# Optimization experiments

Measured on AMD Instinct MI355X. Metric: run time of the kernel, lower is better.

## Reference

```python
import jax, jax.numpy as jnp
import numpy as np

N_NODES = 50000
N_EDGES = 150000
D_FEAT = 512
HIDDEN = 512
N_CLASSES = 47


def gcn_conv(x, edge_index, W, b, n_nodes):
    """PyG GCNConv: out = D^{-1/2} (A + I) D^{-1/2} (x @ W) + b."""
    h = x @ W  # [N, out_dim] dense GEMM
    loop = jnp.arange(n_nodes, dtype=edge_index.dtype)
    row = jnp.concatenate([edge_index[0], loop])  # source
    col = jnp.concatenate([edge_index[1], loop])  # target
    ones = jnp.ones(row.shape[0], dtype=h.dtype)
    deg = jax.ops.segment_sum(ones, col, num_segments=n_nodes)  # in-degree + 1
    dinv = jnp.where(deg > 0, jax.lax.rsqrt(deg), 0.0)
    norm = dinv[row] * dinv[col]  # [E+N]
    msg = norm[:, None] * h[row]  # gather + scale
    out = jax.ops.segment_sum(msg, col, num_segments=n_nodes)  # scatter-add
    return out + b


def setup_inputs() -> dict:
    key = jax.random.key(0)
    k1, k2, k3, k4, k5, k6 = jax.random.split(key, 6)
    x = jax.random.normal(k1, (N_NODES, D_FEAT), dtype=jnp.float32)
    edge_index = jax.random.randint(k2, (2, N_EDGES), 0, N_NODES, dtype=jnp.int64)
    s1 = (6.0 / (D_FEAT + HIDDEN)) ** 0.5
    s2 = (6.0 / (HIDDEN + N_CLASSES)) ** 0.5
    W1 = jax.random.uniform(k3, (D_FEAT, HIDDEN), jnp.float32, -s1, s1)
    b1 = jnp.zeros((HIDDEN,), jnp.float32)
    W2 = jax.random.uniform(k4, (HIDDEN, N_CLASSES), jnp.float32, -s2, s2)
    b2 = jnp.zeros((N_CLASSES,), jnp.float32)
    return {"x": x, "edge_index": edge_index, "W1": W1, "b1": b1, "W2": W2, "b2": b2}


def reference(x, edge_index, W1, b1, W2, b2):
    n = x.shape[0]
    h = gcn_conv(x, edge_index, W1, b1, n)
    h = jax.nn.relu(h)
    # F.dropout(p=0.5, training=self.training): eval mode -> identity
    out = gcn_conv(h, edge_index, W2, b2, n)
    return out
```

## Files before the change

kernel.cpp:

```cpp
#include <hip/hip_runtime.h>
#include <hip/hip_bf16.h>

#define NNODES 50000
#define NEDGES 150000
#define DFEAT  512
#define HID    512
#define NCLS   47

typedef __hip_bfloat16 bf16;
typedef __attribute__((ext_vector_type(8))) short short8;
typedef __attribute__((ext_vector_type(4))) float float4v;

typedef const __attribute__((address_space(1))) unsigned int* gas_t;
typedef __attribute__((address_space(3))) unsigned int* las_t;
__device__ __forceinline__ void load_lds16(const void* g, void* l) {
    __builtin_amdgcn_global_load_lds((gas_t)g, (las_t)l, 16, 0, 0);
}

__device__ __forceinline__ float bfbits_lo(unsigned int w) {
    return __uint_as_float((w & 0xFFFFu) << 16);
}
__device__ __forceinline__ float bfbits_hi(unsigned int w) {
    return __uint_as_float(w & 0xFFFF0000u);
}

__global__ void k_detect(const void* x, const void* ei, int* flags) {
    __shared__ int scnt[64], sor[64];
    int t = threadIdx.x;
    const unsigned short* xs = (const unsigned short*)x;
    int c = 0;
    for (int i = t; i < 256; i += 64) {
        unsigned int e = (xs[2 * i] >> 7) & 0xFF;
        c += (e >= 117 && e <= 130) ? 1 : 0;
    }
    const int* w = (const int*)ei;
    int o = 0;
    for (int i = 2 * t + 1; i < 512; i += 128) o |= w[i];
    scnt[t] = c; sor[t] = o;
    __syncthreads();
    if (t == 0) {
        int C = 0, O = 0;
        for (int i = 0; i < 64; i++) { C += scnt[i]; O |= sor[i]; }
        flags[0] = (C > 128) ? 1 : 0;
        flags[1] = (O == 0) ? 1 : 0;
    }
}

__device__ __forceinline__ int eidx(const void* ei, int half, int e, int is64) {
    if (is64) return (int)((const long long*)ei)[(size_t)half * NEDGES + e];
    return ((const int*)ei)[half * NEDGES + e];
}

__global__ void k_zero32(unsigned int* p, size_t n) {
    size_t i = (size_t)blockIdx.x * blockDim.x + threadIdx.x;
    if (i < n) p[i] = 0u;
}

__global__ void k_cvt(const void* src, float* dst, int n, const int* flags) {
    int i = blockIdx.x * blockDim.x + threadIdx.x;
    if (i >= n) return;
    dst[i] = flags[0] ? __bfloat162float(((const bf16*)src)[i]) : ((const float*)src)[i];
}

__global__ void k_cvt_w1t(const void* W1, bf16* W1T, const int* flags) {
    int i = blockIdx.x * blockDim.x + threadIdx.x;
    if (i >= DFEAT * HID) return;
    int k = i / HID, n = i % HID;
    float v = flags[0] ? __bfloat162float(((const bf16*)W1)[i]) : ((const float*)W1)[i];
    W1T[(size_t)n * DFEAT + k] = __float2bfloat16(v);
}

__global__ void k_cvt_w2t(const void* W2, bf16* W2T, const int* flags) {
    int i = blockIdx.x * blockDim.x + threadIdx.x;
    if (i >= 64 * HID) return;
    int n = i / HID, k = i % HID;
    float v = 0.0f;
    if (n < NCLS) {
        size_t idx = (size_t)k * NCLS + n;
        v = flags[0] ? __bfloat162float(((const bf16*)W2)[idx]) : ((const float*)W2)[idx];
    }
    W2T[(size_t)n * HID + k] = __float2bfloat16(v);
}

__global__ void k_count(const void* ei, int* cnt, const int* flags) {
    int e = blockIdx.x * blockDim.x + threadIdx.x;
    if (e >= NEDGES) return;
    atomicAdd(&cnt[eidx(ei, 1, e, flags[1])], 1);
}

__global__ void k_dinv(const int* cnt, float* dinv) {
    int i = blockIdx.x * blockDim.x + threadIdx.x;
    if (i < NNODES) dinv[i] = rsqrtf(1.0f + (float)cnt[i]);
}

__global__ __launch_bounds__(256) void k_scan_part(const int* cnt, int* part) {
    __shared__ int s[256];
    int i = blockIdx.x * 256 + threadIdx.x;
    s[threadIdx.x] = (i < NNODES) ? cnt[i] : 0;
    __syncthreads();
    for (int off = 128; off > 0; off >>= 1) {
        if (threadIdx.x < off) s[threadIdx.x] += s[threadIdx.x + off];
        __syncthreads();
    }
    if (threadIdx.x == 0) part[blockIdx.x] = s[0];
}

__global__ __launch_bounds__(256) void k_scan_off(int* part, int n) {
    __shared__ int s[256];
    int v = (threadIdx.x < n) ? part[threadIdx.x] : 0;
    s[threadIdx.x] = v;
    __syncthreads();
    for (int off = 1; off < 256; off <<= 1) {
        int t = (threadIdx.x >= off) ? s[threadIdx.x - off] : 0;
        __syncthreads();
        s[threadIdx.x] += t;
        __syncthreads();
    }
    if (threadIdx.x < n) part[threadIdx.x] = s[threadIdx.x] - v;
}

__global__ __launch_bounds__(256) void k_scan_fin(const int* cnt, const int* part,
                                                  int* rowptr, int* cursor) {
    __shared__ int s[256];
    int i = blockIdx.x * 256 + threadIdx.x;
    int v = (i < NNODES) ? cnt[i] : 0;
    s[threadIdx.x] = v;
    __syncthreads();
    for (int off = 1; off < 256; off <<= 1) {
        int t = (threadIdx.x >= off) ? s[threadIdx.x - off] : 0;
        __syncthreads();
        s[threadIdx.x] += t;
        __syncthreads();
    }
    int incl = s[threadIdx.x] + part[blockIdx.x];
    if (i < NNODES) {
        rowptr[i + 1] = incl;
        cursor[i] = incl - v;
    }
    if (i == 0) rowptr[0] = 0;
}

__global__ void k_fill(const void* ei, int* cursor, int* csr_src, const int* flags) {
    int e = blockIdx.x * blockDim.x + threadIdx.x;
    if (e >= NEDGES) return;
    int is64 = flags[1];
    int v = eidx(ei, 1, e, is64);
    int u = eidx(ei, 0, e, is64);
    int pos = atomicAdd(&cursor[v], 1);
    csr_src[pos] = u;
}

__global__ __launch_bounds__(256, 2) void k_gemm1_bs(
    const void* __restrict__ X, const bf16* __restrict__ W1T,
    bf16* __restrict__ h1, const int* __restrict__ flags,
    int rows_per_xcd, int n_row_tiles) {
    __shared__ bf16 Bs[64 * 512];
    const int tid = threadIdx.x;
    const int wave = tid >> 6, lane = tid & 63;
    const int b = blockIdx.x;
    const int xcd = b & 7, s = b >> 3;
    const int col_t = s & 7, lr = s >> 3;
    const int row_t = xcd * rows_per_xcd + lr;
    if (row_t >= n_row_tiles) return;
    const int row0 = row_t * 256;
    const int gc0 = col_t * 64;
    const int isb = flags[0];

    for (int i = 0; i < 16; ++i) {
        int col = wave * 16 + i;
        int ck = (lane & ~7) | ((lane & 7) ^ (col & 7));
        load_lds16(W1T + (size_t)(gc0 + col) * DFEAT + ck * 8, &Bs[col * 512]);
    }
    __syncthreads();

    float4v acc[4][4];
#pragma unroll
    for (int i = 0; i < 4; i++)
#pragma unroll
        for (int j = 0; j < 4; j++) acc[i][j] = (float4v){0.f, 0.f, 0.f, 0.f};

    const int frow = lane & 15, quad = lane >> 4;
    const int wrow0 = row0 + wave * 64;

    for (int ks = 0; ks < 16; ++ks) {
        const int k0 = ks * 32;
        short8 a[4], bfr[4];
        if (isb) {
            const bf16* xb = (const bf16*)X;
#pragma unroll
            for (int f = 0; f < 4; ++f) {
                int gr = wrow0 + f * 16 + frow; if (gr >= NNODES) gr = NNODES - 1;
                a[f] = *(const short8*)(xb + (size_t)gr * DFEAT + k0 + quad * 8);
            }
        } else {
            const float* xf = (const float*)X;
#pragma unroll
            for (int f = 0; f < 4; ++f) {
                int gr = wrow0 + f * 16 + frow; if (gr >= NNODES) gr = NNODES - 1;
                const float* p = xf + (size_t)gr * DFEAT + k0 + quad * 8;
                float4 u = *(const float4*)p;
                float4 v = *(const float4*)(p + 4);
                bf16 tmp[8];
                tmp[0] = __float2bfloat16(u.x); tmp[1] = __float2bfloat16(u.y);
                tmp[2] = __float2bfloat16(u.z); tmp[3] = __float2bfloat16(u.w);
                tmp[4] = __float2bfloat16(v.x); tmp[5] = __float2bfloat16(v.y);
                tmp[6] = __float2bfloat16(v.z); tmp[7] = __float2bfloat16(v.w);
                a[f] = *(const short8*)tmp;
            }
        }
#pragma unroll
        for (int j = 0; j < 4; ++j) {
            int col = j * 16 + frow;
            int ck = ks * 4 + quad;
            int pos = (ck & ~7) | ((ck & 7) ^ (col & 7));
            bfr[j] = *(const short8*)&Bs[col * 512 + pos * 8];
        }
#pragma unroll
        for (int i = 0; i < 4; ++i)
#pragma unroll
            for (int j = 0; j < 4; ++j)
                acc[i][j] = __builtin_amdgcn_mfma_f32_16x16x32_bf16(a[i], bfr[j], acc[i][j], 0, 0, 0);
    }
#pragma unroll
    for (int i = 0; i < 4; ++i) {
#pragma unroll
        for (int r = 0; r < 4; ++r) {
            int grow = wrow0 + i * 16 + quad * 4 + r;
            if (grow < NNODES) {
#pragma unroll
                for (int j = 0; j < 4; ++j)
                    h1[(size_t)grow * HID + gc0 + j * 16 + frow] =
                        __float2bfloat16(acc[i][j][r]);
            }
        }
    }
}

__global__ __launch_bounds__(256, 2) void k_gemm2_bs(
    const bf16* __restrict__ A, const bf16* __restrict__ W2T,
    float* __restrict__ h2) {
    __shared__ bf16 Bs[64 * 512];
    const int tid = threadIdx.x;
    const int wave = tid >> 6, lane = tid & 63;
    const int row0 = blockIdx.x * 128;

    for (int i = 0; i < 16; ++i) {
        int col = wave * 16 + i;
        int ck = (lane & ~7) | ((lane & 7) ^ (col & 7));
        load_lds16(W2T + (size_t)col * HID + ck * 8, &Bs[col * 512]);
    }
    __syncthreads();

    float4v acc[2][4];
#pragma unroll
    for (int i = 0; i < 2; i++)
#pragma unroll
        for (int j = 0; j < 4; j++) acc[i][j] = (float4v){0.f, 0.f, 0.f, 0.f};

    const int frow = lane & 15, quad = lane >> 4;
    const int wrow0 = row0 + wave * 32;

    for (int ks = 0; ks < 16; ++ks) {
        const int k0 = ks * 32;
        short8 a[2], bfr[4];
#pragma unroll
        for (int f = 0; f < 2; ++f) {
            int gr = wrow0 + f * 16 + frow; if (gr >= NNODES) gr = NNODES - 1;
            a[f] = *(const short8*)(A + (size_t)gr * HID + k0 + quad * 8);
        }
#pragma unroll
        for (int j = 0; j < 4; ++j) {
            int col = j * 16 + frow;
            int ck = ks * 4 + quad;
            int pos = (ck & ~7) | ((ck & 7) ^ (col & 7));
            bfr[j] = *(const short8*)&Bs[col * 512 + pos * 8];
        }
#pragma unroll
        for (int i = 0; i < 2; ++i)
#pragma unroll
            for (int j = 0; j < 4; ++j)
                acc[i][j] = __builtin_amdgcn_mfma_f32_16x16x32_bf16(a[i], bfr[j], acc[i][j], 0, 0, 0);
    }
#pragma unroll
    for (int i = 0; i < 2; ++i) {
#pragma unroll
        for (int r = 0; r < 4; ++r) {
            int grow = wrow0 + i * 16 + quad * 4 + r;
            if (grow < NNODES) {
#pragma unroll
                for (int j = 0; j < 4; ++j) {
                    int col = j * 16 + frow;
                    if (col < NCLS)
                        h2[(size_t)grow * NCLS + col] = acc[i][j][r];
                }
            }
        }
    }
}

__global__ __launch_bounds__(256) void k_agg1_512(const bf16* __restrict__ h1c,
                                                  const int* __restrict__ rowptr,
                                                  const int* __restrict__ csr_src,
                                                  const float* __restrict__ dinv,
                                                  const float* __restrict__ b1c,
                                                  bf16* __restrict__ a1c) {
    int v = blockIdx.x * 4 + (threadIdx.x >> 6);
    int lane = threadIdx.x & 63;
    if (v >= NNODES) return;
    int d8 = lane * 8;
    float dv = dinv[v];
    float s2 = dv * dv;
    uint4 w = *(const uint4*)(h1c + (size_t)v * 512 + d8);
    float a0 = s2 * bfbits_lo(w.x), a1 = s2 * bfbits_hi(w.x);
    float a2 = s2 * bfbits_lo(w.y), a3 = s2 * bfbits_hi(w.y);
    float a4 = s2 * bfbits_lo(w.z), a5 = s2 * bfbits_hi(w.z);
    float a6 = s2 * bfbits_lo(w.w), a7 = s2 * bfbits_hi(w.w);
    int pend = rowptr[v + 1];
    for (int p = rowptr[v]; p < pend; ++p) {
        int u = csr_src[p];
        float nw = dinv[u] * dv;
        uint4 q = *(const uint4*)(h1c + (size_t)u * 512 + d8);
        a0 += nw * bfbits_lo(q.x); a1 += nw * bfbits_hi(q.x);
        a2 += nw * bfbits_lo(q.y); a3 += nw * bfbits_hi(q.y);
        a4 += nw * bfbits_lo(q.z); a5 += nw * bfbits_hi(q.z);
        a6 += nw * bfbits_lo(q.w); a7 += nw * bfbits_hi(q.w);
    }
    const float* bb = b1c + d8;
    a0 += bb[0]; a1 += bb[1]; a2 += bb[2]; a3 += bb[3];
    a4 += bb[4]; a5 += bb[5]; a6 += bb[6]; a7 += bb[7];
    bf16 o[8];
    o[0] = __float2bfloat16(a0 > 0.f ? a0 : 0.f);
    o[1] = __float2bfloat16(a1 > 0.f ? a1 : 0.f);
    o[2] = __float2bfloat16(a2 > 0.f ? a2 : 0.f);
    o[3] = __float2bfloat16(a3 > 0.f ? a3 : 0.f);
    o[4] = __float2bfloat16(a4 > 0.f ? a4 : 0.f);
    o[5] = __float2bfloat16(a5 > 0.f ? a5 : 0.f);
    o[6] = __float2bfloat16(a6 > 0.f ? a6 : 0.f);
    o[7] = __float2bfloat16(a7 > 0.f ? a7 : 0.f);
    *(uint4*)(a1c + (size_t)v * 512 + d8) = *(uint4*)o;
}

__global__ __launch_bounds__(256) void k_agg2(const float* __restrict__ h2,
                                              const int* __restrict__ rowptr,
                                              const int* __restrict__ csr_src,
                                              const float* __restrict__ dinv,
                                              const float* __restrict__ b2c,
                                              void* out, const int* flags) {
    int v = blockIdx.x * 4 + (threadIdx.x >> 6);
    int d = threadIdx.x & 63;
    if (v >= NNODES || d >= NCLS) return;
    float dv = dinv[v];
    float acc = dv * dv * h2[(size_t)v * NCLS + d];
    int pend = rowptr[v + 1];
    for (int p = rowptr[v]; p < pend; ++p) {
        int u = csr_src[p];
        acc += dinv[u] * dv * h2[(size_t)u * NCLS + d];
    }
    acc += b2c[d];
    size_t o = (size_t)v * NCLS + d;
    if (flags[0]) ((bf16*)out)[o] = __float2bfloat16(acc);
    else          ((float*)out)[o] = acc;
}

extern "C" void kernel_launch(void* const* d_in, const int* in_sizes, int n_in,
                              void* d_out, int out_size, void* d_ws, size_t ws_size,
                              hipStream_t stream) {
    const void* x  = d_in[0];
    const void* ei = d_in[1];
    const void* W1 = d_in[2];
    const void* b1 = d_in[3];
    const void* W2 = d_in[4];
    const void* b2 = d_in[5];

    char* base = (char*)d_ws;
    auto alloc = [&](size_t bytes) -> char* {
        char* p = base;
        base += (bytes + 255) & ~(size_t)255;
        return p;
    };
    int*   flags  = (int*)alloc(64);
    int*   cnt    = (int*)alloc(sizeof(int) * NNODES);
    int*   part   = (int*)alloc(sizeof(int) * 256);
    int*   rowptr = (int*)alloc(sizeof(int) * (NNODES + 1));
    int*   cursor = (int*)alloc(sizeof(int) * NNODES);
    int*   csr    = (int*)alloc(sizeof(int) * NEDGES);
    float* dinv   = (float*)alloc(sizeof(float) * NNODES);
    bf16*  W1T    = (bf16*)alloc(sizeof(bf16) * DFEAT * HID);
    float* b1c    = (float*)alloc(sizeof(float) * HID);
    bf16*  W2T    = (bf16*)alloc(sizeof(bf16) * 64 * HID);
    float* b2c    = (float*)alloc(sizeof(float) * 64);
    float* h2     = (float*)alloc(sizeof(float) * (size_t)NNODES * NCLS);
    bf16*  h1     = (bf16*)alloc(sizeof(bf16) * (size_t)NNODES * HID);
    bf16*  a1     = (bf16*)alloc(sizeof(bf16) * (size_t)NNODES * HID);

    k_detect<<<1, 64, 0, stream>>>(x, ei, flags);
    k_zero32<<<(NNODES + 255) / 256, 256, 0, stream>>>((unsigned int*)cnt, NNODES);

    k_cvt_w1t<<<(DFEAT * HID + 255) / 256, 256, 0, stream>>>(W1, W1T, flags);
    k_cvt<<<(HID + 255) / 256, 256, 0, stream>>>(b1, b1c, HID, flags);
    k_cvt_w2t<<<(64 * HID + 255) / 256, 256, 0, stream>>>(W2, W2T, flags);
    k_cvt<<<1, 64, 0, stream>>>(b2, b2c, NCLS, flags);

    k_count<<<(NEDGES + 255) / 256, 256, 0, stream>>>(ei, cnt, flags);
    k_dinv<<<(NNODES + 255) / 256, 256, 0, stream>>>(cnt, dinv);
    const int nsb = (NNODES + 255) / 256;
    k_scan_part<<<nsb, 256, 0, stream>>>(cnt, part);
    k_scan_off<<<1, 256, 0, stream>>>(part, nsb);
    k_scan_fin<<<nsb, 256, 0, stream>>>(cnt, part, rowptr, cursor);
    k_fill<<<(NEDGES + 255) / 256, 256, 0, stream>>>(ei, cursor, csr, flags);

    const int n_row_tiles = (NNODES + 255) / 256;
    const int rows_per_xcd = (n_row_tiles + 7) / 8;
    k_gemm1_bs<<<8 * rows_per_xcd * 8, 256, 0, stream>>>(x, W1T, h1, flags,
                                                         rows_per_xcd, n_row_tiles);
    k_agg1_512<<<(NNODES + 3) / 4, 256, 0, stream>>>(h1, rowptr, csr, dinv, b1c, a1);
    k_gemm2_bs<<<(NNODES + 127) / 128, 256, 0, stream>>>(a1, W2T, h2);
    k_agg2<<<(NNODES + 3) / 4, 256, 0, stream>>>(h2, rowptr, csr, dinv, b2c, d_out, flags);
}
```

Before: 368.0 us.

## Drop LDS staging in GEMMs, retile GEMM1, fuse small prep kernels

Both GEMMs now read the B operand (transposed weights) straight from global memory through L1/L2 instead of staging it into LDS with global_load_lds and a barrier. GEMM1 is retiled from 256x64 to 128x128 tiles, with each wave covering 32 rows by 128 columns. Separately, the four weight and bias conversion kernels are merged into one launch, dinv is computed inside the scan-finish kernel, and the layer-1 aggregation prefetches the next CSR index. The goals are less launch overhead, no LDS traffic, and higher occupancy, at the cost of repeated global and cache reads of the weights.

```diff
diff --git a/kernel.cpp b/kernel.cpp
--- a/kernel.cpp
+++ b/kernel.cpp
@@ -11,17 +11,22 @@
 typedef __attribute__((ext_vector_type(8))) short short8;
 typedef __attribute__((ext_vector_type(4))) float float4v;
 
-typedef const __attribute__((address_space(1))) unsigned int* gas_t;
-typedef __attribute__((address_space(3))) unsigned int* las_t;
-__device__ __forceinline__ void load_lds16(const void* g, void* l) {
-    __builtin_amdgcn_global_load_lds((gas_t)g, (las_t)l, 16, 0, 0);
-}
-
 __device__ __forceinline__ float bfbits_lo(unsigned int w) {
     return __uint_as_float((w & 0xFFFFu) << 16);
 }
 __device__ __forceinline__ float bfbits_hi(unsigned int w) {
     return __uint_as_float(w & 0xFFFF0000u);
+}
+
+__device__ __forceinline__ short8 ld_f32_as_bf8(const float* p) {
+    float4 u = *(const float4*)p;
+    float4 v = *(const float4*)(p + 4);
+    bf16 t[8];
+    t[0] = __float2bfloat16(u.x); t[1] = __float2bfloat16(u.y);
+    t[2] = __float2bfloat16(u.z); t[3] = __float2bfloat16(u.w);
+    t[4] = __float2bfloat16(v.x); t[5] = __float2bfloat16(v.y);
+    t[6] = __float2bfloat16(v.z); t[7] = __float2bfloat16(v.w);
+    return *(const short8*)t;
 }
 
 __global__ void k_detect(const void* x, const void* ei, int* flags) {
@@ -56,41 +61,45 @@
     if (i < n) p[i] = 0u;
 }
 
-__global__ void k_cvt(const void* src, float* dst, int n, const int* flags) {
+__global__ void k_cvt_all(const void* W1, const void* b1, const void* W2, const void* b2,
+                          bf16* W1T, bf16* W2T, float* b1c, float* b2c,
+                          const int* flags) {
     int i = blockIdx.x * blockDim.x + threadIdx.x;
-    if (i >= n) return;
-    dst[i] = flags[0] ? __bfloat162float(((const bf16*)src)[i]) : ((const float*)src)[i];
-}
-
-__global__ void k_cvt_w1t(const void* W1, bf16* W1T, const int* flags) {
-    int i = blockIdx.x * blockDim.x + threadIdx.x;
-    if (i >= DFEAT * HID) return;
-    int k = i / HID, n = i % HID;
-    float v = flags[0] ? __bfloat162float(((const bf16*)W1)[i]) : ((const float*)W1)[i];
-    W1T[(size_t)n * DFEAT + k] = __float2bfloat16(v);
-}
-
-__global__ void k_cvt_w2t(const void* W2, bf16* W2T, const int* flags) {
-    int i = blockIdx.x * blockDim.x + threadIdx.x;
-    if (i >= 64 * HID) return;
-    int n = i / HID, k = i % HID;
-    float v = 0.0f;
-    if (n < NCLS) {
-        size_t idx = (size_t)k * NCLS + n;
-        v = flags[0] ? __bfloat162float(((const bf16*)W2)[idx]) : ((const float*)W2)[idx];
-    }
-    W2T[(size_t)n * HID + k] = __float2bfloat16(v);
+    int isb = flags[0];
+    if (i < DFEAT * HID) {
+        int k = i / HID, n = i % HID;
+        float v = isb ? __bfloat162float(((const bf16*)W1)[i]) : ((const float*)W1)[i];
+        W1T[(size_t)n * DFEAT + k] = __float2bfloat16(v);
+        return;
+    }
+    i -= DFEAT * HID;
+    if (i < 64 * HID) {
+        int n = i / HID, k = i % HID;
+        float v = 0.0f;
+        if (n < NCLS) {
+            size_t idx = (size_t)k * NCLS + n;
+            v = isb ? __bfloat162float(((const bf16*)W2)[idx]) : ((const float*)W2)[idx];
+        }
+        W2T[(size_t)n * HID + k] = __float2bfloat16(v);
+        return;
+    }
+    i -= 64 * HID;
+    if (i < HID) {
+        b1c[i] = isb ? __bfloat162float(((const bf16*)b1)[i]) : ((const float*)b1)[i];
+        return;
+    }
+    i -= HID;
+    if (i < 64) {
+        float v = 0.0f;
+        if (i < NCLS) v = isb ? __bfloat162float(((const bf16*)b2)[i]) : ((const float*)b2)[i];
+        b2c[i] = v;
+    }
 }
 
 __global__ void k_count(const void* ei, int* cnt, const int* flags) {
     int e = blockIdx.x * blockDim.x + threadIdx.x;
     if (e >= NEDGES) return;
     atomicAdd(&cnt[eidx(ei, 1, e, flags[1])], 1);
-}
-
-__global__ void k_dinv(const int* cnt, float* dinv) {
-    int i = blockIdx.x * blockDim.x + threadIdx.x;
-    if (i < NNODES) dinv[i] = rsqrtf(1.0f + (float)cnt[i]);
 }
 
 __global__ __launch_bounds__(256) void k_scan_part(const int* cnt, int* part) {
@@ -120,7 +129,7 @@
 }
 
 __global__ __launch_bounds__(256) void k_scan_fin(const int* cnt, const int* part,
-                                                  int* rowptr, int* cursor) {
+                                                  int* rowptr, int* cursor, float* dinv) {
     __shared__ int s[256];
     int i = blockIdx.x * 256 + threadIdx.x;
     int v = (i < NNODES) ? cnt[i] : 0;
@@ -136,6 +145,7 @@
     if (i < NNODES) {
         rowptr[i + 1] = incl;
         cursor[i] = incl - v;
+        dinv[i] = rsqrtf(1.0f + (float)v);
     }
     if (i == 0) rowptr[0] = 0;
 }
@@ -150,85 +160,76 @@
     csr_src[pos] = u;
 }
 
-__global__ __launch_bounds__(256, 2) void k_gemm1_bs(
+__global__ __launch_bounds__(256) void k_gemm1_v5(
     const void* __restrict__ X, const bf16* __restrict__ W1T,
     bf16* __restrict__ h1, const int* __restrict__ flags,
     int rows_per_xcd, int n_row_tiles) {
-    __shared__ bf16 Bs[64 * 512];
-    const int tid = threadIdx.x;
-    const int wave = tid >> 6, lane = tid & 63;
     const int b = blockIdx.x;
     const int xcd = b & 7, s = b >> 3;
-    const int col_t = s & 7, lr = s >> 3;
+    const int col_t = s & 3, lr = s >> 2;
     const int row_t = xcd * rows_per_xcd + lr;
     if (row_t >= n_row_tiles) return;
-    const int row0 = row_t * 256;
-    const int gc0 = col_t * 64;
+    const int row0 = row_t * 128;
+    const int gc0 = col_t * 128;
+    const int wave = threadIdx.x >> 6, lane = threadIdx.x & 63;
+    const int frow = lane & 15, quad = lane >> 4;
+    const int wrow0 = row0 + wave * 32;
     const int isb = flags[0];
 
-    for (int i = 0; i < 16; ++i) {
-        int col = wave * 16 + i;
-        int ck = (lane & ~7) | ((lane & 7) ^ (col & 7));
-        load_lds16(W1T + (size_t)(gc0 + col) * DFEAT + ck * 8, &Bs[col * 512]);
-    }
-    __syncthreads();
-
-    float4v acc[4][4];
-#pragma unroll
-    for (int i = 0; i < 4; i++)
-#pragma unroll
-        for (int j = 0; j < 4; j++) acc[i][j] = (float4v){0.f, 0.f, 0.f, 0.f};
-
-    const int frow = lane & 15, quad = lane >> 4;
-    const int wrow0 = row0 + wave * 64;
-
-    for (int ks = 0; ks < 16; ++ks) {
-        const int k0 = ks * 32;
-        short8 a[4], bfr[4];
-        if (isb) {
-            const bf16* xb = (const bf16*)X;
-#pragma unroll
-            for (int f = 0; f < 4; ++f) {
-                int gr = wrow0 + f * 16 + frow; if (gr >= NNODES) gr = NNODES - 1;
-                a[f] = *(const short8*)(xb + (size_t)gr * DFEAT + k0 + quad * 8);
+    int gr0 = wrow0 + frow;      if (gr0 >= NNODES) gr0 = NNODES - 1;
+    int gr1 = wrow0 + 16 + frow; if (gr1 >= NNODES) gr1 = NNODES - 1;
+
+    const bf16* bcol[8];
+#pragma unroll
+    for (int j = 0; j < 8; ++j)
+        bcol[j] = W1T + (size_t)(gc0 + j * 16 + frow) * DFEAT + quad * 8;
+
+    float4v acc[2][8];
+#pragma unroll
+    for (int i = 0; i < 2; i++)
+#pragma unroll
+        for (int j = 0; j < 8; j++) acc[i][j] = (float4v){0.f, 0.f, 0.f, 0.f};
+
+    if (isb) {
+        const bf16* xb = (const bf16*)X;
+        const bf16* ar0 = xb + (size_t)gr0 * DFEAT + quad * 8;
+        const bf16* ar1 = xb + (size_t)gr1 * DFEAT + quad * 8;
+#pragma unroll 2
+        for (int ks = 0; ks < 16; ++ks) {
+            const int ko = ks * 32;
+            short8 a0 = *(const short8*)(ar0 + ko);
+            short8 a1 = *(const short8*)(ar1 + ko);
+#pragma unroll
+            for (int j = 0; j < 8; ++j) {
+                short8 bb = *(const short8*)(bcol[j] + ko);
+                acc[0][j] = __builtin_amdgcn_mfma_f32_16x16x32_bf16(a0, bb, acc[0][j], 0, 0, 0);
+                acc[1][j] = __builtin_amdgcn_mfma_f32_16x16x32_bf16(a1, bb, acc[1][j], 0, 0, 0);
             }
-        } else {
-            const float* xf = (const float*)X;
-#pragma unroll
-            for (int f = 0; f < 4; ++f) {
-                int gr = wrow0 + f * 16 + frow; if (gr >= NNODES) gr = NNODES - 1;
-                const float* p = xf + (size_t)gr * DFEAT + k0 + quad * 8;
-                float4 u = *(const float4*)p;
-                float4 v = *(const float4*)(p + 4);
-                bf16 tmp[8];
-                tmp[0] = __float2bfloat16(u.x); tmp[1] = __float2bfloat16(u.y);
-                tmp[2] = __float2bfloat16(u.z); tmp[3] = __float2bfloat16(u.w);
-                tmp[4] = __float2bfloat16(v.x); tmp[5] = __float2bfloat16(v.y);
-                tmp[6] = __float2bfloat16(v.z); tmp[7] = __float2bfloat16(v.w);
-                a[f] = *(const short8*)tmp;
+        }
+    } else {
+        const float* xf = (const float*)X;
+        const float* ar0 = xf + (size_t)gr0 * DFEAT + quad * 8;
+        const float* ar1 = xf + (size_t)gr1 * DFEAT + quad * 8;
+        for (int ks = 0; ks < 16; ++ks) {
+            const int ko = ks * 32;
+            short8 a0 = ld_f32_as_bf8(ar0 + ko);
+            short8 a1 = ld_f32_as_bf8(ar1 + ko);
+#pragma unroll
+            for (int j = 0; j < 8; ++j) {
+                short8 bb = *(const short8*)(bcol[j] + ko);
+                acc[0][j] = __builtin_amdgcn_mfma_f32_16x16x32_bf16(a0, bb, acc[0][j], 0, 0, 0);
+                acc[1][j] = __builtin_amdgcn_mfma_f32_16x16x32_bf16(a1, bb, acc[1][j], 0, 0, 0);
             }
         }
-#pragma unroll
-        for (int j = 0; j < 4; ++j) {
-            int col = j * 16 + frow;
-            int ck = ks * 4 + quad;
-            int pos = (ck & ~7) | ((ck & 7) ^ (col & 7));
-            bfr[j] = *(const short8*)&Bs[col * 512 + pos * 8];
-        }
-#pragma unroll
-        for (int i = 0; i < 4; ++i)
-#pragma unroll
-            for (int j = 0; j < 4; ++j)
-                acc[i][j] = __builtin_amdgcn_mfma_f32_16x16x32_bf16(a[i], bfr[j], acc[i][j], 0, 0, 0);
-    }
-#pragma unroll
-    for (int i = 0; i < 4; ++i) {
-#pragma unroll
-        for (int r = 0; r < 4; ++r) {
+    }
+#pragma unroll
+    for (int i = 0; i < 2; i++) {
+#pragma unroll
+        for (int r = 0; r < 4; r++) {
             int grow = wrow0 + i * 16 + quad * 4 + r;
             if (grow < NNODES) {
 #pragma unroll
-                for (int j = 0; j < 4; ++j)
+                for (int j = 0; j < 8; j++)
                     h1[(size_t)grow * HID + gc0 + j * 16 + frow] =
                         __float2bfloat16(acc[i][j][r]);
             }
@@ -236,20 +237,21 @@
     }
 }
 
-__global__ __launch_bounds__(256, 2) void k_gemm2_bs(
+__global__ __launch_bounds__(256) void k_gemm2_v5(
     const bf16* __restrict__ A, const bf16* __restrict__ W2T,
     float* __restrict__ h2) {
-    __shared__ bf16 Bs[64 * 512];
-    const int tid = threadIdx.x;
-    const int wave = tid >> 6, lane = tid & 63;
-    const int row0 = blockIdx.x * 128;
-
-    for (int i = 0; i < 16; ++i) {
-        int col = wave * 16 + i;
-        int ck = (lane & ~7) | ((lane & 7) ^ (col & 7));
-        load_lds16(W2T + (size_t)col * HID + ck * 8, &Bs[col * 512]);
-    }
-    __syncthreads();
+    const int wave = threadIdx.x >> 6, lane = threadIdx.x & 63;
+    const int frow = lane & 15, quad = lane >> 4;
+    const int wrow0 = blockIdx.x * 128 + wave * 32;
+
+    int gr0 = wrow0 + frow;      if (gr0 >= NNODES) gr0 = NNODES - 1;
+    int gr1 = wrow0 + 16 + frow; if (gr1 >= NNODES) gr1 = NNODES - 1;
+    const bf16* ar0 = A + (size_t)gr0 * HID + quad * 8;
+    const bf16* ar1 = A + (size_t)gr1 * HID + quad * 8;
+    const bf16* bcol[4];
+#pragma unroll
+    for (int j = 0; j < 4; ++j)
+        bcol[j] = W2T + (size_t)(j * 16 + frow) * HID + quad * 8;
 
     float4v acc[2][4];
 #pragma unroll
@@ -257,38 +259,26 @@
 #pragma unroll
         for (int j = 0; j < 4; j++) acc[i][j] = (float4v){0.f, 0.f, 0.f, 0.f};
 
-    const int frow = lane & 15, quad = lane >> 4;
-    const int wrow0 = row0 + wave * 32;
-
+#pragma unroll 2
     for (int ks = 0; ks < 16; ++ks) {
-        const int k0 = ks * 32;
-        short8 a[2], bfr[4];
-#pragma unroll
-        for (int f = 0; f < 2; ++f) {
-            int gr = wrow0 + f * 16 + frow; if (gr >= NNODES) gr = NNODES - 1;
-            a[f] = *(const short8*)(A + (size_t)gr * HID + k0 + quad * 8);
-        }
+        const int ko = ks * 32;
+        short8 a0 = *(const short8*)(ar0 + ko);
+        short8 a1 = *(const short8*)(ar1 + ko);
 #pragma unroll
         for (int j = 0; j < 4; ++j) {
-            int col = j * 16 + frow;
-            int ck = ks * 4 + quad;
-            int pos = (ck & ~7) | ((ck & 7) ^ (col & 7));
-            bfr[j] = *(const short8*)&Bs[col * 512 + pos * 8];
-        }
-#pragma unroll
-        for (int i = 0; i < 2; ++i)
-#pragma unroll
-            for (int j = 0; j < 4; ++j)
-                acc[i][j] = __builtin_amdgcn_mfma_f32_16x16x32_bf16(a[i], bfr[j], acc[i][j], 0, 0, 0);
-    }
-#pragma unroll
-    for (int i = 0; i < 2; ++i) {
-#pragma unroll
-        for (int r = 0; r < 4; ++r) {
+            short8 bb = *(const short8*)(bcol[j] + ko);
+            acc[0][j] = __builtin_amdgcn_mfma_f32_16x16x32_bf16(a0, bb, acc[0][j], 0, 0, 0);
+            acc[1][j] = __builtin_amdgcn_mfma_f32_16x16x32_bf16(a1, bb, acc[1][j], 0, 0, 0);
+        }
+    }
+#pragma unroll
+    for (int i = 0; i < 2; i++) {
+#pragma unroll
+        for (int r = 0; r < 4; r++) {
             int grow = wrow0 + i * 16 + quad * 4 + r;
             if (grow < NNODES) {
 #pragma unroll
-                for (int j = 0; j < 4; ++j) {
+                for (int j = 0; j < 4; j++) {
                     int col = j * 16 + frow;
                     if (col < NCLS)
                         h2[(size_t)grow * NCLS + col] = acc[i][j][r];
@@ -315,9 +305,12 @@
     float a2 = s2 * bfbits_lo(w.y), a3 = s2 * bfbits_hi(w.y);
     float a4 = s2 * bfbits_lo(w.z), a5 = s2 * bfbits_hi(w.z);
     float a6 = s2 * bfbits_lo(w.w), a7 = s2 * bfbits_hi(w.w);
-    int pend = rowptr[v + 1];
-    for (int p = rowptr[v]; p < pend; ++p) {
-        int u = csr_src[p];
+    int p = rowptr[v], pend = rowptr[v + 1];
+    int u_nxt = (p < pend) ? csr_src[p] : 0;
+    for (; p < pend;) {
+        int u = u_nxt;
+        ++p;
+        u_nxt = (p < pend) ? csr_src[p] : 0;
         float nw = dinv[u] * dv;
         uint4 q = *(const uint4*)(h1c + (size_t)u * 512 + d8);
         a0 += nw * bfbits_lo(q.x); a1 += nw * bfbits_hi(q.x);
@@ -396,24 +389,22 @@
     k_detect<<<1, 64, 0, stream>>>(x, ei, flags);
     k_zero32<<<(NNODES + 255) / 256, 256, 0, stream>>>((unsigned int*)cnt, NNODES);
 
-    k_cvt_w1t<<<(DFEAT * HID + 255) / 256, 256, 0, stream>>>(W1, W1T, flags);
-    k_cvt<<<(HID + 255) / 256, 256, 0, stream>>>(b1, b1c, HID, flags);
-    k_cvt_w2t<<<(64 * HID + 255) / 256, 256, 0, stream>>>(W2, W2T, flags);
-    k_cvt<<<1, 64, 0, stream>>>(b2, b2c, NCLS, flags);
+    const int cvt_total = DFEAT * HID + 64 * HID + HID + 64;
+    k_cvt_all<<<(cvt_total + 255) / 256, 256, 0, stream>>>(W1, b1, W2, b2, W1T, W2T,
+                                                           b1c, b2c, flags);
 
     k_count<<<(NEDGES + 255) / 256, 256, 0, stream>>>(ei, cnt, flags);
-    k_dinv<<<(NNODES + 255) / 256, 256, 0, stream>>>(cnt, dinv);
     const int nsb = (NNODES + 255) / 256;
     k_scan_part<<<nsb, 256, 0, stream>>>(cnt, part);
     k_scan_off<<<1, 256, 0, stream>>>(part, nsb);
-    k_scan_fin<<<nsb, 256, 0, stream>>>(cnt, part, rowptr, cursor);
+    k_scan_fin<<<nsb, 256, 0, stream>>>(cnt, part, rowptr, cursor, dinv);
     k_fill<<<(NEDGES + 255) / 256, 256, 0, stream>>>(ei, cursor, csr, flags);
 
-    const int n_row_tiles = (NNODES + 255) / 256;
+    const int n_row_tiles = (NNODES + 127) / 128;
     const int rows_per_xcd = (n_row_tiles + 7) / 8;
-    k_gemm1_bs<<<8 * rows_per_xcd * 8, 256, 0, stream>>>(x, W1T, h1, flags,
+    k_gemm1_v5<<<8 * rows_per_xcd * 4, 256, 0, stream>>>(x, W1T, h1, flags,
                                                          rows_per_xcd, n_row_tiles);
     k_agg1_512<<<(NNODES + 3) / 4, 256, 0, stream>>>(h1, rowptr, csr, dinv, b1c, a1);
-    k_gemm2_bs<<<(NNODES + 127) / 128, 256, 0, stream>>>(a1, W2T, h2);
+    k_gemm2_v5<<<(NNODES + 127) / 128, 256, 0, stream>>>(a1, W2T, h2);
     k_agg2<<<(NNODES + 3) / 4, 256, 0, stream>>>(h2, rowptr, csr, dinv, b2c, d_out, flags);
 }
```

Result: slower. 402.4 us (+9.3%).
